# Optimization experiments

Measured on AMD Instinct MI355X. Metric: run time of the kernel, lower is better.

The kernel has to match this reference:

```python
import jax, jax.numpy as jnp
import numpy as np

N, E, D_IN, D_H, G = 20000, 320000, 512, 256, 128


def setup_inputs() -> dict:
    key = jax.random.key(0)
    ks = jax.random.split(key, 9)
    x = jax.random.normal(ks[0], (N, D_IN), dtype=jnp.float32)
    edge_index = jax.random.randint(ks[1], (2, E), 0, N, dtype=jnp.int32)
    batch = jnp.sort(jax.random.randint(ks[2], (N,), 0, G, dtype=jnp.int32))
    W1 = jax.random.normal(ks[3], (D_IN, D_H), dtype=jnp.float32) / np.float32(np.sqrt(D_IN))
    b1 = jnp.zeros((D_H,), dtype=jnp.float32)
    W2 = jax.random.normal(ks[4], (D_H, D_H), dtype=jnp.float32) / np.float32(np.sqrt(D_H))
    b2 = jnp.zeros((D_H,), dtype=jnp.float32)
    w_fc = jax.random.normal(ks[5], (D_H, 1), dtype=jnp.float32) / np.float32(np.sqrt(D_H))
    b_fc = jnp.zeros((1,), dtype=jnp.float32)
    return {"x": x, "edge_index": edge_index, "batch": batch,
            "W1": W1, "b1": b1, "W2": W2, "b2": b2, "w_fc": w_fc, "b_fc": b_fc}


def gcn_conv(x, W, b, src, dst, n):
    # PyG GCNConv: out = D^{-1/2} (A+I) D^{-1/2} (X W) + b  (self-loops already in src/dst)
    xw = x @ W                                            # [n, d_out]
    deg = jnp.zeros((n,), xw.dtype).at[dst].add(1.0)       # in-degree incl. self loop
    dinv = jnp.where(deg > 0, jax.lax.rsqrt(deg), 0.0)
    coef = (dinv[src] * dinv[dst])[:, None]               # [e, 1]
    out = jnp.zeros_like(xw).at[dst].add(xw[src] * coef)  # gather-scale-scatter
    return out + b


def reference(x, edge_index, batch, W1, b1, W2, b2, w_fc, b_fc):
    n = x.shape[0]
    loops = jnp.arange(n, dtype=edge_index.dtype)
    src = jnp.concatenate([edge_index[0], loops])
    dst = jnp.concatenate([edge_index[1], loops])
    h = jax.nn.relu(gcn_conv(x, W1, b1, src, dst, n))
    h = jax.nn.relu(gcn_conv(h, W2, b2, src, dst, n))
    # global_mean_pool over graph ids
    sums = jax.ops.segment_sum(h, batch, num_segments=G)                      # [G, d]
    cnt = jax.ops.segment_sum(jnp.ones((n, 1), h.dtype), batch, num_segments=G)
    pooled = sums / jnp.maximum(cnt, 1.0)
    return (pooled @ w_fc + b_fc)[:, 0]                                       # [G]
```

## Files before the change

### kernel.cpp

```cpp
#include <hip/hip_runtime.h>
#include <hip/hip_fp16.h>


#define TPB 256
#define CAP 64

typedef _Float16 hfrag __attribute__((ext_vector_type(8)));
typedef float f32x4 __attribute__((ext_vector_type(4)));

__global__ __launch_bounds__(TPB) void k_init(int* __restrict__ cursor, int N,
                                              const float* __restrict__ W1,
                                              unsigned short* __restrict__ B1,
                                              int K1,
                                              const float* __restrict__ W2,
                                              unsigned short* __restrict__ B2h,
                                              unsigned short* __restrict__ B2l,
                                              int K2) {
  int nbz = (N + TPB - 1) / TPB;
  int b = blockIdx.x;
  if (b < nbz) {
    int i = b * TPB + threadIdx.x;
    if (i < N) cursor[i] = 0;
    return;
  }
  int t = (b - nbz) * TPB + threadIdx.x;
  if (t < K1 * 256) {
    int n = t & 255, k = t >> 8;
    float v = W1[(size_t)k * 256 + n];
    __half h = __float2half(v);
    B1[((size_t)(k >> 5) * 256 + n) * 32 + (k & 31)] = *(unsigned short*)&h;
  } else {
    t -= K1 * 256;
    if (t >= K2 * 256) return;
    int n = t & 255, k = t >> 8;
    float v = W2[(size_t)k * 256 + n];
    __half h = __float2half(v);
    __half l = __float2half(v - __half2float(h));
    size_t o = ((size_t)(k >> 5) * 256 + n) * 32 + (k & 31);
    B2h[o] = *(unsigned short*)&h;
    B2l[o] = *(unsigned short*)&l;
  }
}

#define LDSTR 72

template <int MODE>
__device__ __forceinline__ void gemm_core(const unsigned short* __restrict__ Bph,
                                          const unsigned short* __restrict__ Bpl,
                                          __half* __restrict__ C, int M, int K,
                                          int bm, int bn,
                                          unsigned short (*AsH)[LDSTR],
                                          unsigned short (*AsL)[LDSTR],
                                          const float* A_f32,
                                          const __half* A_f16) {
  const int tid = threadIdx.x;
  const int w = tid >> 6;
  const int lane = tid & 63;
  const int q = lane >> 4;
  const int nin = lane & 15;
  const int r  = tid >> 2;
  const int cb = (tid & 3) << 4;
  const int row = bm + r;
  const bool rok = row < M;

  size_t bbase[2];
#pragma unroll
  for (int nt = 0; nt < 2; ++nt)
    bbase[nt] = ((size_t)(bn + w * 32 + nt * 16 + nin)) * 32 + q * 8;

  f32x4 acc[4][2];
#pragma unroll
  for (int mt = 0; mt < 4; ++mt)
#pragma unroll
    for (int nt = 0; nt < 2; ++nt) acc[mt][nt] = (f32x4){0.f, 0.f, 0.f, 0.f};

  float4 rf[4];
  uint4  rh[2];
  if (MODE == 0) {
    rf[0] = make_float4(0.f, 0.f, 0.f, 0.f); rf[1] = rf[0]; rf[2] = rf[0]; rf[3] = rf[0];
    if (rok) {
      const float* Ap = A_f32 + (size_t)row * K + cb;
      rf[0] = *(const float4*)(Ap);
      rf[1] = *(const float4*)(Ap + 4);
      rf[2] = *(const float4*)(Ap + 8);
      rf[3] = *(const float4*)(Ap + 12);
    }
  } else {
    rh[0] = make_uint4(0, 0, 0, 0); rh[1] = rh[0];
    if (rok) {
      const __half* Ap = A_f16 + (size_t)row * K + cb;
      rh[0] = *(const uint4*)(Ap);
      rh[1] = *(const uint4*)(Ap + 8);
    }
  }

  for (int kb = 0; kb < K; kb += 64) {
    if (MODE == 0) {
      float vv[16];
      *(float4*)&vv[0] = rf[0]; *(float4*)&vv[4] = rf[1];
      *(float4*)&vv[8] = rf[2]; *(float4*)&vv[12] = rf[3];
      unsigned short h16[16], l16[16];
#pragma unroll
      for (int j = 0; j < 16; ++j) {
        __half h = __float2half(vv[j]);
        __half l = __float2half(vv[j] - __half2float(h));
        h16[j] = *(unsigned short*)&h;
        l16[j] = *(unsigned short*)&l;
      }
      __syncthreads();
      *(uint4*)&AsH[r][cb]     = *(uint4*)&h16[0];
      *(uint4*)&AsH[r][cb + 8] = *(uint4*)&h16[8];
      *(uint4*)&AsL[r][cb]     = *(uint4*)&l16[0];
      *(uint4*)&AsL[r][cb + 8] = *(uint4*)&l16[8];
      __syncthreads();
    } else {
      __syncthreads();
      *(uint4*)&AsH[r][cb]     = rh[0];
      *(uint4*)&AsH[r][cb + 8] = rh[1];
      __syncthreads();
    }

    int kn = kb + 64;
    if (kn < K && rok) {
      if (MODE == 0) {
        const float* Ap = A_f32 + (size_t)row * K + kn + cb;
        rf[0] = *(const float4*)(Ap);
        rf[1] = *(const float4*)(Ap + 4);
        rf[2] = *(const float4*)(Ap + 8);
        rf[3] = *(const float4*)(Ap + 12);
      } else {
        const __half* Ap = A_f16 + (size_t)row * K + kn + cb;
        rh[0] = *(const uint4*)(Ap);
        rh[1] = *(const uint4*)(Ap + 8);
      }
    }

#pragma unroll
    for (int s = 0; s < 2; ++s) {
      const size_t koff = (size_t)((kb >> 5) + s) * 256 * 32;
      if (MODE == 0) {
        hfrag bh[2];
#pragma unroll
        for (int nt = 0; nt < 2; ++nt)
          bh[nt] = *(const hfrag*)(Bph + koff + bbase[nt]);
        hfrag ah[4], al[4];
#pragma unroll
        for (int mt = 0; mt < 4; ++mt) {
          ah[mt] = *(const hfrag*)&AsH[mt * 16 + nin][s * 32 + q * 8];
          al[mt] = *(const hfrag*)&AsL[mt * 16 + nin][s * 32 + q * 8];
        }
#pragma unroll
        for (int mt = 0; mt < 4; ++mt)
#pragma unroll
          for (int nt = 0; nt < 2; ++nt) {
            acc[mt][nt] = __builtin_amdgcn_mfma_f32_16x16x32_f16(ah[mt], bh[nt], acc[mt][nt], 0, 0, 0);
            acc[mt][nt] = __builtin_amdgcn_mfma_f32_16x16x32_f16(al[mt], bh[nt], acc[mt][nt], 0, 0, 0);
          }
      } else {
        hfrag bh[2], bl[2];
#pragma unroll
        for (int nt = 0; nt < 2; ++nt) {
          bh[nt] = *(const hfrag*)(Bph + koff + bbase[nt]);
          bl[nt] = *(const hfrag*)(Bpl + koff + bbase[nt]);
        }
        hfrag a4[4];
#pragma unroll
        for (int mt = 0; mt < 4; ++mt)
          a4[mt] = *(const hfrag*)&AsH[mt * 16 + nin][s * 32 + q * 8];
#pragma unroll
        for (int mt = 0; mt < 4; ++mt)
#pragma unroll
          for (int nt = 0; nt < 2; ++nt) {
            acc[mt][nt] = __builtin_amdgcn_mfma_f32_16x16x32_f16(a4[mt], bh[nt], acc[mt][nt], 0, 0, 0);
            acc[mt][nt] = __builtin_amdgcn_mfma_f32_16x16x32_f16(a4[mt], bl[nt], acc[mt][nt], 0, 0, 0);
          }
      }
    }
  }

#pragma unroll
  for (int mt = 0; mt < 4; ++mt) {
    int rb = bm + mt * 16 + q * 4;
#pragma unroll
    for (int reg = 0; reg < 4; ++reg) {
      int rr = rb + reg;
      if (rr < M) {
#pragma unroll
        for (int nt = 0; nt < 2; ++nt)
          C[(size_t)rr * 256 + bn + w * 32 + nt * 16 + nin] = __float2half(acc[mt][nt][reg]);
      }
    }
  }
}

__global__ __launch_bounds__(TPB) void k_gemm1_scatter(const float* __restrict__ A,
                                                       const unsigned short* __restrict__ Bph,
                                                       __half* __restrict__ C, int M, int K,
                                                       const int* __restrict__ src,
                                                       const int* __restrict__ dst,
                                                       int* __restrict__ cursor,
                                                       unsigned* __restrict__ pairw, int E) {
  __shared__ unsigned short AsH[64][LDSTR];
  __shared__ unsigned short AsL[64][LDSTR];
  int nbg = 2 * ((M + 63) / 64);
  int b = blockIdx.x;
  if (b < nbg) {
    gemm_core<0>(Bph, nullptr, C, M, K, (b >> 1) * 64, (b & 1) * 128, AsH, AsL, A, nullptr);
    return;
  }
  int e = (b - nbg) * TPB + threadIdx.x;
  if (e >= E) return;
  int s = src[e], d = dst[e];
  int pos = d * CAP + atomicAdd(&cursor[d], 1);
  pairw[pos] = (unsigned)s;
}

__global__ __launch_bounds__(TPB) void k_gemm2(const __half* __restrict__ A,
                                               const unsigned short* __restrict__ Bph,
                                               const unsigned short* __restrict__ Bpl,
                                               __half* __restrict__ C, int M, int K) {
  __shared__ unsigned short AsH[64][LDSTR];
  gemm_core<1>(Bph, Bpl, C, M, K, blockIdx.y * 64, blockIdx.x * 128, AsH, nullptr, nullptr, A);
}

__device__ __forceinline__ f32x4 gather_row4(const uint2* __restrict__ xq,
                                             const unsigned* __restrict__ pairw,
                                             const int* __restrict__ cnt,
                                             int node, int deg, float ci, int lane) {
  f32x4 a = (f32x4){0.f, 0.f, 0.f, 0.f};
  int base = node * CAP;
  int k = 0;
  for (; k + 7 < deg; k += 8) {
#pragma unroll
    for (int u = 0; u < 8; ++u) {
      int j = (int)pairw[base + k + u];
      float coef = rsqrtf(ci * (float)(cnt[j] + 1));
      uint2 v = (xq + ((size_t)j << 6))[lane];
      float2 f0 = __half22float2(*(__half2*)&v.x);
      float2 f1 = __half22float2(*(__half2*)&v.y);
      a[0] = fmaf(coef, f0.x, a[0]);
      a[1] = fmaf(coef, f0.y, a[1]);
      a[2] = fmaf(coef, f1.x, a[2]);
      a[3] = fmaf(coef, f1.y, a[3]);
    }
  }
  for (; k < deg; ++k) {
    int j = (int)pairw[base + k];
    float coef = rsqrtf(ci * (float)(cnt[j] + 1));
    uint2 v = (xq + ((size_t)j << 6))[lane];
    float2 f0 = __half22float2(*(__half2*)&v.x);
    float2 f1 = __half22float2(*(__half2*)&v.y);
    a[0] = fmaf(coef, f0.x, a[0]);
    a[1] = fmaf(coef, f0.y, a[1]);
    a[2] = fmaf(coef, f1.x, a[2]);
    a[3] = fmaf(coef, f1.y, a[3]);
  }
  return a;
}

__global__ __launch_bounds__(TPB) void k_gather1(const uint2* __restrict__ xq,
                                                 const int* __restrict__ cnt,
                                                 const unsigned* __restrict__ pairw,
                                                 const float* __restrict__ bias,
                                                 uint2* __restrict__ h1, int N) {
  int node = __builtin_amdgcn_readfirstlane(blockIdx.x * 4 + (threadIdx.x >> 6));
  if (node >= N) return;
  int deg = __builtin_amdgcn_readfirstlane(cnt[node]);
  int lane = threadIdx.x & 63;
  float ci = (float)(deg + 1);
  f32x4 acc = gather_row4(xq, pairw, cnt, node, deg, ci, lane);
  float di2 = 1.f / ci;
  uint2 sv = xq[((size_t)node << 6) + lane];
  float2 s0 = __half22float2(*(__half2*)&sv.x);
  float2 s1 = __half22float2(*(__half2*)&sv.y);
  acc[0] = fmaf(di2, s0.x, acc[0]);
  acc[1] = fmaf(di2, s0.y, acc[1]);
  acc[2] = fmaf(di2, s1.x, acc[2]);
  acc[3] = fmaf(di2, s1.y, acc[3]);
  const float4 bb = *(const float4*)&bias[4 * lane];
  float r0 = fmaxf(acc[0] + bb.x, 0.f);
  float r1 = fmaxf(acc[1] + bb.y, 0.f);
  float r2 = fmaxf(acc[2] + bb.z, 0.f);
  float r3 = fmaxf(acc[3] + bb.w, 0.f);
  __half2 o0 = __floats2half2_rn(r0, r1);
  __half2 o1 = __floats2half2_rn(r2, r3);
  uint2 o;
  o.x = *(unsigned*)&o0;
  o.y = *(unsigned*)&o1;
  h1[((size_t)node << 6) + lane] = o;
}

__global__ __launch_bounds__(TPB) void k_gather2(const uint2* __restrict__ xq,
                                                 const int* __restrict__ cnt,
                                                 const unsigned* __restrict__ pairw,
                                                 const float* __restrict__ bias,
                                                 const float* __restrict__ wfc,
                                                 float* __restrict__ pdot, int N) {
  int node = __builtin_amdgcn_readfirstlane(blockIdx.x * 4 + (threadIdx.x >> 6));
  if (node >= N) return;
  int deg = __builtin_amdgcn_readfirstlane(cnt[node]);
  int lane = threadIdx.x & 63;
  float ci = (float)(deg + 1);
  f32x4 acc = gather_row4(xq, pairw, cnt, node, deg, ci, lane);
  float di2 = 1.f / ci;
  uint2 sv = xq[((size_t)node << 6) + lane];
  float2 s0 = __half22float2(*(__half2*)&sv.x);
  float2 s1 = __half22float2(*(__half2*)&sv.y);
  acc[0] = fmaf(di2, s0.x, acc[0]);
  acc[1] = fmaf(di2, s0.y, acc[1]);
  acc[2] = fmaf(di2, s1.x, acc[2]);
  acc[3] = fmaf(di2, s1.y, acc[3]);
  const float4 bb = *(const float4*)&bias[4 * lane];
  const float4 ff = *(const float4*)&wfc[4 * lane];
  float s = fmaxf(acc[0] + bb.x, 0.f) * ff.x + fmaxf(acc[1] + bb.y, 0.f) * ff.y +
            fmaxf(acc[2] + bb.z, 0.f) * ff.z + fmaxf(acc[3] + bb.w, 0.f) * ff.w;
#pragma unroll
  for (int off = 32; off > 0; off >>= 1) s += __shfl_down(s, off);
  if (lane == 0) pdot[node] = s;
}

__global__ __launch_bounds__(TPB) void k_pool(const float* __restrict__ pdot,
                                              const int* __restrict__ batch,
                                              const float* __restrict__ bfc,
                                              float* __restrict__ out, int N) {
  int g = blockIdx.x;
  int lo = 0, hi = N;
  while (lo < hi) { int mid = (lo + hi) >> 1; if (batch[mid] < g) lo = mid + 1; else hi = mid; }
  int start = lo;
  hi = N;
  while (lo < hi) { int mid = (lo + hi) >> 1; if (batch[mid] < g + 1) lo = mid + 1; else hi = mid; }
  int end = lo;

  float s = 0.f;
  for (int i = start + threadIdx.x; i < end; i += TPB) s += pdot[i];
  __shared__ float red[4];
  int lane = threadIdx.x & 63, wave = threadIdx.x >> 6;
#pragma unroll
  for (int off = 32; off > 0; off >>= 1) s += __shfl_down(s, off);
  if (lane == 0) red[wave] = s;
  __syncthreads();
  if (threadIdx.x == 0) {
    float tot = red[0] + red[1] + red[2] + red[3];
    float c = (float)(end - start);
    out[g] = tot / fmaxf(c, 1.f) + bfc[0];
  }
}

extern "C" void kernel_launch(void* const* d_in, const int* in_sizes, int n_in,
                              void* d_out, int out_size, void* d_ws, size_t ws_size,
                              hipStream_t stream) {
  const float* x    = (const float*)d_in[0];
  const int*   eidx = (const int*)d_in[1];
  const int*   batch= (const int*)d_in[2];
  const float* W1   = (const float*)d_in[3];
  const float* b1   = (const float*)d_in[4];
  const float* W2   = (const float*)d_in[5];
  const float* b2   = (const float*)d_in[6];
  const float* wfc  = (const float*)d_in[7];
  const float* bfc  = (const float*)d_in[8];
  float* out = (float*)d_out;

  const int N  = in_sizes[2];
  const int E  = in_sizes[1] / 2;
  const int K1 = in_sizes[0] / N;
  const int G  = out_size;

  const int* srcp = eidx;
  const int* dstp = eidx + E;

  auto al16 = [](size_t v) { return (v + 15) & ~(size_t)15; };
  char* ws = (char*)d_ws;
  size_t off = 0;
  int*      cursor = (int*)(ws + off);         off = al16(off + (size_t)N * 4);
  unsigned* pairw  = (unsigned*)(ws + off);    off = al16(off + (size_t)N * CAP * 4);
  float*    pdot   = (float*)(ws + off);       off = al16(off + (size_t)N * 4);
  __half*   bufH   = (__half*)(ws + off);      off = al16(off + (size_t)N * 256 * 2);
  __half*   h1f    = (__half*)(ws + off);      off = al16(off + (size_t)N * 256 * 2);
  unsigned short* W1h = (unsigned short*)(ws + off); off = al16(off + (size_t)K1 * 256 * 2);
  unsigned short* W2h = (unsigned short*)(ws + off); off = al16(off + (size_t)256 * 256 * 2);
  unsigned short* W2l = (unsigned short*)(ws + off); off = al16(off + (size_t)256 * 256 * 2);

  const int nbz = (N + TPB - 1) / TPB;
  const int nbW = ((K1 + 256) * 256 + TPB - 1) / TPB;
  const int nbE = (E + TPB - 1) / TPB;
  const int nbg = 2 * ((N + 63) / 64);
  const int nbG = (N + 3) / 4;
  const dim3 g2(2, (N + 63) / 64);

  k_init<<<nbz + nbW, TPB, 0, stream>>>(cursor, N, W1, W1h, K1, W2, W2h, W2l, 256);

  k_gemm1_scatter<<<nbg + nbE, TPB, 0, stream>>>(x, W1h, bufH, N, K1,
                                                 srcp, dstp, cursor, pairw, E);
  k_gather1<<<nbG, TPB, 0, stream>>>((const uint2*)bufH, cursor, pairw, b1,
                                     (uint2*)h1f, N);

  k_gemm2<<<g2, TPB, 0, stream>>>(h1f, W2h, W2l, bufH, N, 256);
  k_gather2<<<nbG, TPB, 0, stream>>>((const uint2*)bufH, cursor, pairw, b2,
                                     wfc, pdot, N);

  k_pool<<<G, TPB, 0, stream>>>(pdot, batch, bfc, out, N);
}
```

Baseline: 193.0 us.

## Drop split-fp16 GEMM compensation, cache edge coefficients, fuse gather2 with pooling

Both GEMMs drop the hi/lo fp16 split and use a single fp16 operand, which halves the MFMA count and the LDS traffic at the cost of accuracy. After the first gather, each node's edge list is rewritten to hold the source index and a precomputed fp16 normalisation coefficient, so the second gather no longer reads neighbour degrees or computes rsqrt. The second gather and the mean pool are fused: per-node dot products are atomically added into per-graph sums, and the last block to finish computes the outputs. This removes one kernel launch and the pdot buffer. Packing the index into 16 bits limits node indices to 65535, and the fp16 coefficients and operands lose precision.

```diff
diff --git a/kernel.cpp b/kernel.cpp
--- a/kernel.cpp
+++ b/kernel.cpp
@@ -9,48 +9,43 @@
 typedef float f32x4 __attribute__((ext_vector_type(4)));
 
 __global__ __launch_bounds__(TPB) void k_init(int* __restrict__ cursor, int N,
+                                              float* __restrict__ gsum,
+                                              int* __restrict__ done, int G,
                                               const float* __restrict__ W1,
-                                              unsigned short* __restrict__ B1,
-                                              int K1,
+                                              unsigned short* __restrict__ B1, int K1,
                                               const float* __restrict__ W2,
-                                              unsigned short* __restrict__ B2h,
-                                              unsigned short* __restrict__ B2l,
-                                              int K2) {
+                                              unsigned short* __restrict__ B2, int K2) {
   int nbz = (N + TPB - 1) / TPB;
   int b = blockIdx.x;
   if (b < nbz) {
     int i = b * TPB + threadIdx.x;
     if (i < N) cursor[i] = 0;
+    if (b == 0) {
+      if ((int)threadIdx.x < G) gsum[threadIdx.x] = 0.f;
+      if (threadIdx.x == 0) *done = 0;
+    }
     return;
   }
   int t = (b - nbz) * TPB + threadIdx.x;
-  if (t < K1 * 256) {
-    int n = t & 255, k = t >> 8;
-    float v = W1[(size_t)k * 256 + n];
-    __half h = __float2half(v);
-    B1[((size_t)(k >> 5) * 256 + n) * 32 + (k & 31)] = *(unsigned short*)&h;
-  } else {
+  const float* W = W1;
+  unsigned short* B = B1;
+  if (t >= K1 * 256) {
     t -= K1 * 256;
     if (t >= K2 * 256) return;
-    int n = t & 255, k = t >> 8;
-    float v = W2[(size_t)k * 256 + n];
-    __half h = __float2half(v);
-    __half l = __float2half(v - __half2float(h));
-    size_t o = ((size_t)(k >> 5) * 256 + n) * 32 + (k & 31);
-    B2h[o] = *(unsigned short*)&h;
-    B2l[o] = *(unsigned short*)&l;
-  }
+    W = W2; B = B2;
+  }
+  int n = t & 255, k = t >> 8;
+  __half h = __float2half(W[(size_t)k * 256 + n]);
+  B[((size_t)(k >> 5) * 256 + n) * 32 + (k & 31)] = *(unsigned short*)&h;
 }
 
 #define LDSTR 72
 
 template <int MODE>
-__device__ __forceinline__ void gemm_core(const unsigned short* __restrict__ Bph,
-                                          const unsigned short* __restrict__ Bpl,
+__device__ __forceinline__ void gemm_core(const unsigned short* __restrict__ Bp,
                                           __half* __restrict__ C, int M, int K,
                                           int bm, int bn,
-                                          unsigned short (*AsH)[LDSTR],
-                                          unsigned short (*AsL)[LDSTR],
+                                          unsigned short (*As)[LDSTR],
                                           const float* A_f32,
                                           const __half* A_f16) {
   const int tid = threadIdx.x;
@@ -99,24 +94,20 @@
       float vv[16];
       *(float4*)&vv[0] = rf[0]; *(float4*)&vv[4] = rf[1];
       *(float4*)&vv[8] = rf[2]; *(float4*)&vv[12] = rf[3];
-      unsigned short h16[16], l16[16];
+      unsigned short h16[16];
 #pragma unroll
       for (int j = 0; j < 16; ++j) {
         __half h = __float2half(vv[j]);
-        __half l = __float2half(vv[j] - __half2float(h));
         h16[j] = *(unsigned short*)&h;
-        l16[j] = *(unsigned short*)&l;
       }
       __syncthreads();
-      *(uint4*)&AsH[r][cb]     = *(uint4*)&h16[0];
-      *(uint4*)&AsH[r][cb + 8] = *(uint4*)&h16[8];
-      *(uint4*)&AsL[r][cb]     = *(uint4*)&l16[0];
-      *(uint4*)&AsL[r][cb + 8] = *(uint4*)&l16[8];
+      *(uint4*)&As[r][cb]     = *(uint4*)&h16[0];
+      *(uint4*)&As[r][cb + 8] = *(uint4*)&h16[8];
       __syncthreads();
     } else {
       __syncthreads();
-      *(uint4*)&AsH[r][cb]     = rh[0];
-      *(uint4*)&AsH[r][cb + 8] = rh[1];
+      *(uint4*)&As[r][cb]     = rh[0];
+      *(uint4*)&As[r][cb + 8] = rh[1];
       __syncthreads();
     }
 
@@ -138,43 +129,19 @@
 #pragma unroll
     for (int s = 0; s < 2; ++s) {
       const size_t koff = (size_t)((kb >> 5) + s) * 256 * 32;
-      if (MODE == 0) {
-        hfrag bh[2];
+      hfrag bf[2];
+#pragma unroll
+      for (int nt = 0; nt < 2; ++nt)
+        bf[nt] = *(const hfrag*)(Bp + koff + bbase[nt]);
+      hfrag af[4];
+#pragma unroll
+      for (int mt = 0; mt < 4; ++mt)
+        af[mt] = *(const hfrag*)&As[mt * 16 + nin][s * 32 + q * 8];
+#pragma unroll
+      for (int mt = 0; mt < 4; ++mt)
 #pragma unroll
         for (int nt = 0; nt < 2; ++nt)
-          bh[nt] = *(const hfrag*)(Bph + koff + bbase[nt]);
-        hfrag ah[4], al[4];
-#pragma unroll
-        for (int mt = 0; mt < 4; ++mt) {
-          ah[mt] = *(const hfrag*)&AsH[mt * 16 + nin][s * 32 + q * 8];
-          al[mt] = *(const hfrag*)&AsL[mt * 16 + nin][s * 32 + q * 8];
-        }
-#pragma unroll
-        for (int mt = 0; mt < 4; ++mt)
-#pragma unroll
-          for (int nt = 0; nt < 2; ++nt) {
-            acc[mt][nt] = __builtin_amdgcn_mfma_f32_16x16x32_f16(ah[mt], bh[nt], acc[mt][nt], 0, 0, 0);
-            acc[mt][nt] = __builtin_amdgcn_mfma_f32_16x16x32_f16(al[mt], bh[nt], acc[mt][nt], 0, 0, 0);
-          }
-      } else {
-        hfrag bh[2], bl[2];
-#pragma unroll
-        for (int nt = 0; nt < 2; ++nt) {
-          bh[nt] = *(const hfrag*)(Bph + koff + bbase[nt]);
-          bl[nt] = *(const hfrag*)(Bpl + koff + bbase[nt]);
-        }
-        hfrag a4[4];
-#pragma unroll
-        for (int mt = 0; mt < 4; ++mt)
-          a4[mt] = *(const hfrag*)&AsH[mt * 16 + nin][s * 32 + q * 8];
-#pragma unroll
-        for (int mt = 0; mt < 4; ++mt)
-#pragma unroll
-          for (int nt = 0; nt < 2; ++nt) {
-            acc[mt][nt] = __builtin_amdgcn_mfma_f32_16x16x32_f16(a4[mt], bh[nt], acc[mt][nt], 0, 0, 0);
-            acc[mt][nt] = __builtin_amdgcn_mfma_f32_16x16x32_f16(a4[mt], bl[nt], acc[mt][nt], 0, 0, 0);
-          }
-      }
+          acc[mt][nt] = __builtin_amdgcn_mfma_f32_16x16x32_f16(af[mt], bf[nt], acc[mt][nt], 0, 0, 0);
     }
   }
 
@@ -194,18 +161,17 @@
 }
 
 __global__ __launch_bounds__(TPB) void k_gemm1_scatter(const float* __restrict__ A,
-                                                       const unsigned short* __restrict__ Bph,
+                                                       const unsigned short* __restrict__ Bp,
                                                        __half* __restrict__ C, int M, int K,
                                                        const int* __restrict__ src,
                                                        const int* __restrict__ dst,
                                                        int* __restrict__ cursor,
                                                        unsigned* __restrict__ pairw, int E) {
-  __shared__ unsigned short AsH[64][LDSTR];
-  __shared__ unsigned short AsL[64][LDSTR];
+  __shared__ unsigned short As[64][LDSTR];
   int nbg = 2 * ((M + 63) / 64);
   int b = blockIdx.x;
   if (b < nbg) {
-    gemm_core<0>(Bph, nullptr, C, M, K, (b >> 1) * 64, (b & 1) * 128, AsH, AsL, A, nullptr);
+    gemm_core<0>(Bp, C, M, K, (b >> 1) * 64, (b & 1) * 128, As, A, nullptr);
     return;
   }
   int e = (b - nbg) * TPB + threadIdx.x;
@@ -216,26 +182,25 @@
 }
 
 __global__ __launch_bounds__(TPB) void k_gemm2(const __half* __restrict__ A,
-                                               const unsigned short* __restrict__ Bph,
-                                               const unsigned short* __restrict__ Bpl,
+                                               const unsigned short* __restrict__ Bp,
                                                __half* __restrict__ C, int M, int K) {
-  __shared__ unsigned short AsH[64][LDSTR];
-  gemm_core<1>(Bph, Bpl, C, M, K, blockIdx.y * 64, blockIdx.x * 128, AsH, nullptr, nullptr, A);
-}
-
-__device__ __forceinline__ f32x4 gather_row4(const uint2* __restrict__ xq,
-                                             const unsigned* __restrict__ pairw,
-                                             const int* __restrict__ cnt,
-                                             int node, int deg, float ci, int lane) {
+  __shared__ unsigned short As[64][LDSTR];
+  gemm_core<1>(Bp, C, M, K, blockIdx.y * 64, blockIdx.x * 128, As, nullptr, A);
+}
+
+__device__ __forceinline__ f32x4 gather_row4p(const uint2* __restrict__ xq,
+                                              const unsigned* __restrict__ pairw,
+                                              int node, int deg, int lane) {
   f32x4 a = (f32x4){0.f, 0.f, 0.f, 0.f};
   int base = node * CAP;
   int k = 0;
   for (; k + 7 < deg; k += 8) {
 #pragma unroll
     for (int u = 0; u < 8; ++u) {
-      int j = (int)pairw[base + k + u];
-      float coef = rsqrtf(ci * (float)(cnt[j] + 1));
-      uint2 v = (xq + ((size_t)j << 6))[lane];
+      unsigned uu = pairw[base + k + u];
+      unsigned short cb16 = (unsigned short)(uu & 0xFFFFu);
+      float coef = __half2float(*(__half*)&cb16);
+      uint2 v = (xq + ((size_t)(uu >> 16) << 6))[lane];
       float2 f0 = __half22float2(*(__half2*)&v.x);
       float2 f1 = __half22float2(*(__half2*)&v.y);
       a[0] = fmaf(coef, f0.x, a[0]);
@@ -245,9 +210,10 @@
     }
   }
   for (; k < deg; ++k) {
-    int j = (int)pairw[base + k];
-    float coef = rsqrtf(ci * (float)(cnt[j] + 1));
-    uint2 v = (xq + ((size_t)j << 6))[lane];
+    unsigned uu = pairw[base + k];
+    unsigned short cb16 = (unsigned short)(uu & 0xFFFFu);
+    float coef = __half2float(*(__half*)&cb16);
+    uint2 v = (xq + ((size_t)(uu >> 16) << 6))[lane];
     float2 f0 = __half22float2(*(__half2*)&v.x);
     float2 f1 = __half22float2(*(__half2*)&v.y);
     a[0] = fmaf(coef, f0.x, a[0]);
@@ -260,15 +226,45 @@
 
 __global__ __launch_bounds__(TPB) void k_gather1(const uint2* __restrict__ xq,
                                                  const int* __restrict__ cnt,
-                                                 const unsigned* __restrict__ pairw,
+                                                 unsigned* __restrict__ pairw,
                                                  const float* __restrict__ bias,
                                                  uint2* __restrict__ h1, int N) {
   int node = __builtin_amdgcn_readfirstlane(blockIdx.x * 4 + (threadIdx.x >> 6));
   if (node >= N) return;
   int deg = __builtin_amdgcn_readfirstlane(cnt[node]);
   int lane = threadIdx.x & 63;
+  int base = node * CAP;
   float ci = (float)(deg + 1);
-  f32x4 acc = gather_row4(xq, pairw, cnt, node, deg, ci, lane);
+
+  f32x4 acc = (f32x4){0.f, 0.f, 0.f, 0.f};
+  {
+    int k = 0;
+    for (; k + 7 < deg; k += 8) {
+#pragma unroll
+      for (int u = 0; u < 8; ++u) {
+        int j = (int)pairw[base + k + u];
+        float coef = rsqrtf(ci * (float)(cnt[j] + 1));
+        uint2 v = (xq + ((size_t)j << 6))[lane];
+        float2 f0 = __half22float2(*(__half2*)&v.x);
+        float2 f1 = __half22float2(*(__half2*)&v.y);
+        acc[0] = fmaf(coef, f0.x, acc[0]);
+        acc[1] = fmaf(coef, f0.y, acc[1]);
+        acc[2] = fmaf(coef, f1.x, acc[2]);
+        acc[3] = fmaf(coef, f1.y, acc[3]);
+      }
+    }
+    for (; k < deg; ++k) {
+      int j = (int)pairw[base + k];
+      float coef = rsqrtf(ci * (float)(cnt[j] + 1));
+      uint2 v = (xq + ((size_t)j << 6))[lane];
+      float2 f0 = __half22float2(*(__half2*)&v.x);
+      float2 f1 = __half22float2(*(__half2*)&v.y);
+      acc[0] = fmaf(coef, f0.x, acc[0]);
+      acc[1] = fmaf(coef, f0.y, acc[1]);
+      acc[2] = fmaf(coef, f1.x, acc[2]);
+      acc[3] = fmaf(coef, f1.y, acc[3]);
+    }
+  }
   float di2 = 1.f / ci;
   uint2 sv = xq[((size_t)node << 6) + lane];
   float2 s0 = __half22float2(*(__half2*)&sv.x);
@@ -288,61 +284,67 @@
   o.x = *(unsigned*)&o0;
   o.y = *(unsigned*)&o1;
   h1[((size_t)node << 6) + lane] = o;
-}
-
-__global__ __launch_bounds__(TPB) void k_gather2(const uint2* __restrict__ xq,
-                                                 const int* __restrict__ cnt,
-                                                 const unsigned* __restrict__ pairw,
-                                                 const float* __restrict__ bias,
-                                                 const float* __restrict__ wfc,
-                                                 float* __restrict__ pdot, int N) {
-  int node = __builtin_amdgcn_readfirstlane(blockIdx.x * 4 + (threadIdx.x >> 6));
-  if (node >= N) return;
-  int deg = __builtin_amdgcn_readfirstlane(cnt[node]);
-  int lane = threadIdx.x & 63;
-  float ci = (float)(deg + 1);
-  f32x4 acc = gather_row4(xq, pairw, cnt, node, deg, ci, lane);
-  float di2 = 1.f / ci;
-  uint2 sv = xq[((size_t)node << 6) + lane];
-  float2 s0 = __half22float2(*(__half2*)&sv.x);
-  float2 s1 = __half22float2(*(__half2*)&sv.y);
-  acc[0] = fmaf(di2, s0.x, acc[0]);
-  acc[1] = fmaf(di2, s0.y, acc[1]);
-  acc[2] = fmaf(di2, s1.x, acc[2]);
-  acc[3] = fmaf(di2, s1.y, acc[3]);
-  const float4 bb = *(const float4*)&bias[4 * lane];
-  const float4 ff = *(const float4*)&wfc[4 * lane];
-  float s = fmaxf(acc[0] + bb.x, 0.f) * ff.x + fmaxf(acc[1] + bb.y, 0.f) * ff.y +
-            fmaxf(acc[2] + bb.z, 0.f) * ff.z + fmaxf(acc[3] + bb.w, 0.f) * ff.w;
-#pragma unroll
-  for (int off = 32; off > 0; off >>= 1) s += __shfl_down(s, off);
-  if (lane == 0) pdot[node] = s;
-}
-
-__global__ __launch_bounds__(TPB) void k_pool(const float* __restrict__ pdot,
-                                              const int* __restrict__ batch,
-                                              const float* __restrict__ bfc,
-                                              float* __restrict__ out, int N) {
-  int g = blockIdx.x;
-  int lo = 0, hi = N;
-  while (lo < hi) { int mid = (lo + hi) >> 1; if (batch[mid] < g) lo = mid + 1; else hi = mid; }
-  int start = lo;
-  hi = N;
-  while (lo < hi) { int mid = (lo + hi) >> 1; if (batch[mid] < g + 1) lo = mid + 1; else hi = mid; }
-  int end = lo;
-
-  float s = 0.f;
-  for (int i = start + threadIdx.x; i < end; i += TPB) s += pdot[i];
-  __shared__ float red[4];
-  int lane = threadIdx.x & 63, wave = threadIdx.x >> 6;
-#pragma unroll
-  for (int off = 32; off > 0; off >>= 1) s += __shfl_down(s, off);
-  if (lane == 0) red[wave] = s;
+
+  if (lane < deg) {
+    int j = (int)pairw[base + lane];
+    float coef = rsqrtf(ci * (float)(cnt[j] + 1));
+    __half hc = __float2half(coef);
+    pairw[base + lane] = ((unsigned)j << 16) | (unsigned)(*(unsigned short*)&hc);
+  }
+}
+
+__global__ __launch_bounds__(TPB) void k_gather2_pool(const uint2* __restrict__ xq,
+                                                      const int* __restrict__ cnt,
+                                                      const unsigned* __restrict__ pairw,
+                                                      const float* __restrict__ bias,
+                                                      const float* __restrict__ wfc,
+                                                      const int* __restrict__ batch,
+                                                      const float* __restrict__ bfc,
+                                                      float* __restrict__ gsum,
+                                                      int* __restrict__ done,
+                                                      float* __restrict__ out,
+                                                      int N, int G) {
+  __shared__ int lastFlag;
+  int tid = threadIdx.x;
+  int lane = tid & 63;
+  int node = blockIdx.x * 4 + (tid >> 6);
+  if (node < N) {
+    node = __builtin_amdgcn_readfirstlane(node);
+    int deg = __builtin_amdgcn_readfirstlane(cnt[node]);
+    f32x4 acc = gather_row4p(xq, pairw, node, deg, lane);
+    float di2 = 1.f / (float)(deg + 1);
+    uint2 sv = xq[((size_t)node << 6) + lane];
+    float2 s0 = __half22float2(*(__half2*)&sv.x);
+    float2 s1 = __half22float2(*(__half2*)&sv.y);
+    acc[0] = fmaf(di2, s0.x, acc[0]);
+    acc[1] = fmaf(di2, s0.y, acc[1]);
+    acc[2] = fmaf(di2, s1.x, acc[2]);
+    acc[3] = fmaf(di2, s1.y, acc[3]);
+    const float4 bb = *(const float4*)&bias[4 * lane];
+    const float4 ff = *(const float4*)&wfc[4 * lane];
+    float s = fmaxf(acc[0] + bb.x, 0.f) * ff.x + fmaxf(acc[1] + bb.y, 0.f) * ff.y +
+              fmaxf(acc[2] + bb.z, 0.f) * ff.z + fmaxf(acc[3] + bb.w, 0.f) * ff.w;
+#pragma unroll
+    for (int off = 32; off > 0; off >>= 1) s += __shfl_down(s, off);
+    if (lane == 0) atomicAdd(&gsum[batch[node]], s);
+  }
   __syncthreads();
-  if (threadIdx.x == 0) {
-    float tot = red[0] + red[1] + red[2] + red[3];
-    float c = (float)(end - start);
-    out[g] = tot / fmaxf(c, 1.f) + bfc[0];
+  if (tid == 0) {
+    __threadfence();
+    int t = atomicAdd(done, 1);
+    lastFlag = (t == (int)gridDim.x - 1) ? 1 : 0;
+  }
+  __syncthreads();
+  if (lastFlag && tid < G) {
+    int g = tid;
+    int lo = 0, hi = N;
+    while (lo < hi) { int m = (lo + hi) >> 1; if (batch[m] < g) lo = m + 1; else hi = m; }
+    int start = lo;
+    hi = N;
+    while (lo < hi) { int m = (lo + hi) >> 1; if (batch[m] < g + 1) lo = m + 1; else hi = m; }
+    float c = (float)(lo - start);
+    float sg = atomicAdd(&gsum[g], 0.f);
+    out[g] = sg / fmaxf(c, 1.f) + bfc[0];
   }
 }
 
@@ -373,12 +375,12 @@
   size_t off = 0;
   int*      cursor = (int*)(ws + off);         off = al16(off + (size_t)N * 4);
   unsigned* pairw  = (unsigned*)(ws + off);    off = al16(off + (size_t)N * CAP * 4);
-  float*    pdot   = (float*)(ws + off);       off = al16(off + (size_t)N * 4);
+  float*    gsum   = (float*)(ws + off);       off = al16(off + (size_t)G * 4);
+  int*      done   = (int*)(ws + off);         off = al16(off + 16);
   __half*   bufH   = (__half*)(ws + off);      off = al16(off + (size_t)N * 256 * 2);
   __half*   h1f    = (__half*)(ws + off);      off = al16(off + (size_t)N * 256 * 2);
   unsigned short* W1h = (unsigned short*)(ws + off); off = al16(off + (size_t)K1 * 256 * 2);
   unsigned short* W2h = (unsigned short*)(ws + off); off = al16(off + (size_t)256 * 256 * 2);
-  unsigned short* W2l = (unsigned short*)(ws + off); off = al16(off + (size_t)256 * 256 * 2);
 
   const int nbz = (N + TPB - 1) / TPB;
   const int nbW = ((K1 + 256) * 256 + TPB - 1) / TPB;
@@ -387,16 +389,16 @@
   const int nbG = (N + 3) / 4;
   const dim3 g2(2, (N + 63) / 64);
 
-  k_init<<<nbz + nbW, TPB, 0, stream>>>(cursor, N, W1, W1h, K1, W2, W2h, W2l, 256);
+  k_init<<<nbz + nbW, TPB, 0, stream>>>(cursor, N, gsum, done, G,
+                                        W1, W1h, K1, W2, W2h, 256);
 
   k_gemm1_scatter<<<nbg + nbE, TPB, 0, stream>>>(x, W1h, bufH, N, K1,
                                                  srcp, dstp, cursor, pairw, E);
   k_gather1<<<nbG, TPB, 0, stream>>>((const uint2*)bufH, cursor, pairw, b1,
                                      (uint2*)h1f, N);
 
-  k_gemm2<<<g2, TPB, 0, stream>>>(h1f, W2h, W2l, bufH, N, 256);
-  k_gather2<<<nbG, TPB, 0, stream>>>((const uint2*)bufH, cursor, pairw, b2,
-                                     wfc, pdot, N);
-
-  k_pool<<<G, TPB, 0, stream>>>(pdot, batch, bfc, out, N);
-}
+  k_gemm2<<<g2, TPB, 0, stream>>>(h1f, W2h, bufH, N, 256);
+
+  k_gather2_pool<<<nbG, TPB, 0, stream>>>((const uint2*)bufH, cursor, pairw, b2,
+                                          wfc, batch, bfc, gsum, done, out, N, G);
+}
```

Result: slower. 352.9 us (+82.9%).
